# Performance work log

Measured on AMD Instinct MI355X. Metric: run time of the kernel, lower is better.

## Reference

```python
import jax, jax.numpy as jnp
import numpy as np

D = 128          # embed_dim
NSYM = 100000    # num_symbols
PAD = NSYM       # padding idx (zero row)
B = 2048         # query batch
FEW = 5          # support set size
M = 128          # max neighbors
KTAB = 64        # knn table width
K = 32           # knn_k topk
STEPS = 4        # process_steps
DM = 2 * D       # d_model for encoders (256)
HID = 2 * DM     # LSTM hidden (512)


def _cos(a, b):
    # torch F.cosine_similarity, eps=1e-8; a [B,1,d], b [B,N,d] -> [B,N]
    num = jnp.sum(a * b, axis=-1)
    den = jnp.maximum(jnp.linalg.norm(a, axis=-1) * jnp.linalg.norm(b, axis=-1), 1e-8)
    return num / den


def _l2n(x):
    return x / jnp.maximum(jnp.linalg.norm(x, axis=-1, keepdims=True), 1e-12)


def _neighbor_encoder(conn, ids, knn_tab, emb, gcn_w, gcn_w_b, gcn_b, gate_w, gate_b):
    rel = emb[conn[..., 0]]                      # [N,M,D]
    ent = emb[conn[..., 1]]                      # [N,M,D]
    center = emb[ids][:, None, :]                # [N,1,D]
    sim = _cos(center, ent)                      # [N,M]
    _, idx = jax.lax.top_k(sim, K)               # [N,K]
    rel_k = jnp.take_along_axis(rel, idx[..., None], axis=1)
    ent_k = jnp.take_along_axis(ent, idx[..., None], axis=1)
    h = jnp.concatenate([rel_k, ent_k], axis=-1) @ gcn_w.T + gcn_w_b + gcn_b
    struct = jnp.tanh(h.mean(axis=1))            # [N,D]
    # knn branch: gather knn neighbor ids, cosine topk, pad-relation embeds (zero row)
    kent = emb[knn_tab[ids]]                     # [N,KTAB,D]
    sim2 = _cos(center, kent)
    _, idx2 = jax.lax.top_k(sim2, K)
    kent_k = jnp.take_along_axis(kent, idx2[..., None], axis=1)
    pad_row = jax.lax.stop_gradient(emb[PAD])    # padding_idx row (zeros, no grad)
    krel = jnp.broadcast_to(pad_row, kent_k.shape)
    h2 = jnp.concatenate([krel, kent_k], axis=-1) @ gcn_w.T + gcn_w_b + gcn_b
    knn_mean = jnp.tanh(h2.mean(axis=1))         # [N,D]
    alpha = jax.nn.sigmoid(jnp.concatenate([struct, knn_mean], axis=-1) @ gate_w.T + gate_b)
    return (1.0 - alpha) * struct + alpha * knn_mean


def _support_encoder(x, p1_w, p1_b, p2_w, p2_b, ln_g, ln_b):
    o = jax.nn.relu(x @ p1_w.T + p1_b) @ p2_w.T + p2_b
    z = o + x
    mu = z.mean(axis=-1, keepdims=True)
    sig = z.std(axis=-1, ddof=1, keepdims=True)  # torch unbiased std
    return (z - mu) / (sig + 1e-3) * ln_g + ln_b


def _query_encoder(support, query, w_ih, w_hh, b_ih, b_hh):
    # attLSTM processing block; support [1,DM], query [B,DM]
    n = query.shape[0]
    h_r = jnp.zeros((n, HID), query.dtype)
    c = jnp.zeros((n, HID), query.dtype)
    h = query
    for _ in range(STEPS):
        g = query @ w_ih.T + b_ih + h_r @ w_hh.T + b_hh
        i, f, gg, o = jnp.split(g, 4, axis=-1)
        c = jax.nn.sigmoid(f) * c + jax.nn.sigmoid(i) * jnp.tanh(gg)
        h_ = jax.nn.sigmoid(o) * jnp.tanh(c)
        h = query + h_[:, :DM]
        attn = jax.nn.softmax(h @ support.T, axis=1)  # [B,1]
        r = attn @ support                             # [B,DM]
        h_r = jnp.concatenate([h, r], axis=1)
    return h


def _forward(query, support, q_l_conn, q_r_conn, s_l_conn, s_r_conn, knn_neighbors,
             emb, gcn_w, gcn_w_b, gcn_b, gate_w, gate_b,
             p1_w, p1_b, p2_w, p2_b, ln_g, ln_b, w_ih, w_hh, b_ih, b_hh):
    ne = lambda conn, ids: _neighbor_encoder(conn, ids, knn_neighbors, emb,
                                             gcn_w, gcn_w_b, gcn_b, gate_w, gate_b)
    ql = ne(q_l_conn, query[:, 0])
    qr = ne(q_r_conn, query[:, 1])
    sl = ne(s_l_conn, support[:, 0])
    sr = ne(s_r_conn, support[:, 1])
    qn = jnp.concatenate([ql, qr], axis=-1)   # [B,DM]
    sn = jnp.concatenate([sl, sr], axis=-1)   # [FEW,DM]
    se = lambda x: _support_encoder(x, p1_w, p1_b, p2_w, p2_b, ln_g, ln_b)
    support_g = se(sn).mean(axis=0, keepdims=True)  # [1,DM]
    query_g = se(qn)                                 # [B,DM]
    query_f = _l2n(_query_encoder(support_g, query_g, w_ih, w_hh, b_ih, b_hh))
    sg = _l2n(support_g[0])
    return query_f @ sg                              # [B]


def setup_inputs() -> dict:
    key = jax.random.key(0)
    ks = jax.random.split(key, 24)
    f = lambda i, shape, s=0.05: jax.random.normal(ks[i], shape, dtype=jnp.float32) * s
    ri = lambda i, shape: jax.random.randint(ks[i], shape, 0, NSYM).astype(jnp.int32)
    emb = f(0, (NSYM + 1, D), 0.5).at[PAD].set(0.0)
    return dict(
        query=ri(1, (B, 2)), support=ri(2, (FEW, 2)),
        q_l_conn=ri(3, (B, M, 2)),
        q_l_deg=jax.random.randint(ks[4], (B,), 1, M).astype(jnp.int32),
        q_r_conn=ri(5, (B, M, 2)),
        q_r_deg=jax.random.randint(ks[6], (B,), 1, M).astype(jnp.int32),
        s_l_conn=ri(7, (FEW, M, 2)),
        s_l_deg=jax.random.randint(ks[8], (FEW,), 1, M).astype(jnp.int32),
        s_r_conn=ri(9, (FEW, M, 2)),
        s_r_deg=jax.random.randint(ks[10], (FEW,), 1, M).astype(jnp.int32),
        knn_neighbors=ri(11, (NSYM + 1, KTAB)),
        emb=emb,
        gcn_w=f(12, (D, 2 * D)), gcn_w_b=f(13, (D,)),
        gcn_b=jnp.zeros((D,), jnp.float32),
        gate_w=f(14, (1, 2 * D)), gate_b=jnp.zeros((1,), jnp.float32),
        p1_w=f(15, (2 * DM, DM)), p1_b=f(16, (2 * DM,)),
        p2_w=f(17, (DM, 2 * DM)), p2_b=f(18, (DM,)),
        ln_g=jnp.ones((DM,), jnp.float32), ln_b=jnp.zeros((DM,), jnp.float32),
        w_ih=f(19, (4 * HID, DM)), w_hh=f(20, (4 * HID, HID)),
        b_ih=f(21, (4 * HID,)), b_hh=f(22, (4 * HID,)),
    )


def reference(query, support, q_l_conn, q_l_deg, q_r_conn, q_r_deg,
              s_l_conn, s_l_deg, s_r_conn, s_r_deg, knn_neighbors,
              emb, gcn_w, gcn_w_b, gcn_b, gate_w, gate_b,
              p1_w, p1_b, p2_w, p2_b, ln_g, ln_b, w_ih, w_hh, b_ih, b_hh):
    # degrees are computed-but-unused in this fork's neighbor_encoder (plain mean)
    return _forward(query, support, q_l_conn, q_r_conn, s_l_conn, s_r_conn, knn_neighbors,
                    emb, gcn_w, gcn_w_b, gcn_b, gate_w, gate_b,
                    p1_w, p1_b, p2_w, p2_b, ln_g, ln_b, w_ih, w_hh, b_ih, b_hh)
```

## Files before the change

### kernel.cpp

```cpp
#include <hip/hip_runtime.h>
#include <hip/hip_bf16.h>

typedef unsigned short u16;
typedef unsigned int u32;

constexpr int ED   = 128;
constexpr int MC   = 128;
constexpr int KT   = 64;
constexpr int KS   = 32;
constexpr int NB   = 2048;
constexpr int NF   = 5;
constexpr int DMM  = 256;
constexpr int NG   = 1024;
constexpr int PADID = 100000;
constexpr int NROWS = 2*NB + 2*NF;
constexpr int MT   = (NROWS + 63)/64;
constexpr int MP   = MT*64;

typedef __attribute__((ext_vector_type(8))) short short8;
typedef __attribute__((ext_vector_type(4))) float floatx4;

__device__ __forceinline__ float bf2f(u16 u){
  union { u32 i; float f; } v; v.i = ((u32)u) << 16; return v.f;
}
__device__ __forceinline__ float lo2f(u32 w){
  union { u32 i; float f; } v; v.i = w << 16; return v.f;
}
__device__ __forceinline__ float hi2f(u32 w){
  union { u32 i; float f; } v; v.i = w & 0xffff0000u; return v.f;
}
__device__ __forceinline__ u16 f2bf(float f){
  union { float f; u32 i; } v; v.f = f;
  u32 r = v.i + 0x7FFFu + ((v.i >> 16) & 1u);
  return (u16)(r >> 16);
}
__device__ __forceinline__ float sigf(float x){ return 1.f / (1.f + expf(-x)); }

__device__ __forceinline__ bool sniff(const void* ln_g){
  return *(const u32*)ln_g == 0x3F803F80u;
}

__device__ __forceinline__ float gld(const void* p, size_t i, bool bf){
  return bf ? bf2f(((const u16*)p)[i]) : ((const float*)p)[i];
}
__device__ __forceinline__ void ld4(const void* p, size_t i0, bool bf, float* o){
  if (bf){ uint2 w = *(const uint2*)((const u16*)p + i0);
           o[0]=lo2f(w.x); o[1]=hi2f(w.x); o[2]=lo2f(w.y); o[3]=hi2f(w.y); }
  else   { float4 v = *(const float4*)((const float*)p + i0);
           o[0]=v.x; o[1]=v.y; o[2]=v.z; o[3]=v.w; }
}
__device__ __forceinline__ void ld8(const void* p, size_t i0, bool bf, float* o){
  if (bf){
    uint4 v = *(const uint4*)((const u16*)p + i0);
    o[0]=lo2f(v.x); o[1]=hi2f(v.x); o[2]=lo2f(v.y); o[3]=hi2f(v.y);
    o[4]=lo2f(v.z); o[5]=hi2f(v.z); o[6]=lo2f(v.w); o[7]=hi2f(v.w);
  } else {
    const float* f = (const float*)p + i0;
    float4 a = *(const float4*)f, b = *(const float4*)(f + 4);
    o[0]=a.x; o[1]=a.y; o[2]=a.z; o[3]=a.w; o[4]=b.x; o[5]=b.y; o[6]=b.z; o[7]=b.w;
  }
}
__device__ __forceinline__ float dotw(const void* w, size_t i0, const float* x, int n, bool bf){
  float acc = 0.f, t[8];
  #pragma unroll 4
  for (int j = 0; j < n; j += 8){
    ld8(w, i0 + j, bf, t);
    #pragma unroll
    for (int q = 0; q < 8; q++) acc += t[q]*x[j+q];
  }
  return acc;
}

__device__ __forceinline__ float waveSum(float v){
  #pragma unroll
  for (int o = 32; o > 0; o >>= 1) v += __shfl_xor(v, o, 64);
  return v;
}
__device__ __forceinline__ float blockSum(float v, float* s8){
  int lane = threadIdx.x & 63, wid = threadIdx.x >> 6;
  v = waveSum(v);
  __syncthreads();
  if (lane == 0) s8[wid] = v;
  __syncthreads();
  return s8[0] + s8[1] + s8[2] + s8[3];
}
__device__ __forceinline__ float2 blockSum2(float a, float b, float* s8){
  int lane = threadIdx.x & 63, wid = threadIdx.x >> 6;
  a = waveSum(a); b = waveSum(b);
  __syncthreads();
  if (lane == 0){ s8[wid] = a; s8[4 + wid] = b; }
  __syncthreads();
  float2 r;
  r.x = s8[0] + s8[1] + s8[2] + s8[3];
  r.y = s8[4] + s8[5] + s8[6] + s8[7];
  return r;
}

__global__ __launch_bounds__(256) void neighbor_kernel(
    const int* __restrict__ query, const int* __restrict__ support,
    const int* __restrict__ qlc, const int* __restrict__ qrc,
    const int* __restrict__ slc, const int* __restrict__ srcc,
    const int* __restrict__ knnt, const void* __restrict__ emb,
    float* __restrict__ gA, float* __restrict__ gK, const void* __restrict__ ln_g)
{
  const bool bf = sniff(ln_g);
  int blk = blockIdx.x;
  const int* conn; int id;
  if (blk < NB)            { id = query[2*blk];                 conn = qlc + (size_t)blk*MC*2; }
  else if (blk < 2*NB)     { int r = blk - NB;   id = query[2*r+1];   conn = qrc + (size_t)r*MC*2; }
  else if (blk < 2*NB+NF)  { int r = blk - 2*NB; id = support[2*r];   conn = slc + (size_t)r*MC*2; }
  else                     { int r = blk - 2*NB - NF; id = support[2*r+1]; conn = srcc + (size_t)r*MC*2; }

  __shared__ float s_center[ED];
  __shared__ float s_sim[MC + KT];
  __shared__ float s_red[8];
  __shared__ int s_eid[MC + KT];
  __shared__ int s_selE[KS], s_selR[KS], s_selK[KS];

  const int tid = threadIdx.x, lane = tid & 63, wid = tid >> 6;

  if (tid < ED) s_center[tid] = gld(emb, (size_t)id*ED + tid, bf);
  if (tid < MC)           s_eid[tid] = conn[2*tid + 1];
  else if (tid < MC + KT) s_eid[tid] = knnt[(size_t)id*KT + (tid - MC)];

  float cpart = 0.f;
  if (tid < ED){ float c = s_center[tid]; cpart = c*c; }
  float cnorm = sqrtf(blockSum(cpart, s_red));

  const int g = lane & 15;
  float creg[8];
  #pragma unroll
  for (int j = 0; j < 8; j++) creg[j] = s_center[g*8 + j];

  #pragma unroll 4
  for (int m0 = wid*4; m0 < MC + KT; m0 += 16){
    int m = m0 + (lane >> 4);
    int eid = s_eid[m];
    float e[8];
    ld8(emb, (size_t)eid*ED + g*8, bf, e);
    float d = 0.f, q = 0.f;
    #pragma unroll
    for (int j = 0; j < 8; j++){ d += creg[j]*e[j]; q += e[j]*e[j]; }
    #pragma unroll
    for (int o = 8; o > 0; o >>= 1){ d += __shfl_xor(d, o, 64); q += __shfl_xor(q, o, 64); }
    if (g == 0) s_sim[m] = d / fmaxf(cnorm * sqrtf(q), 1e-8f);
  }
  __syncthreads();

  if (tid < MC){
    float v = s_sim[tid];
    int cnt = 0;
    #pragma unroll 8
    for (int j = 0; j < MC; j++){
      float w = s_sim[j];
      cnt += (w > v || (w == v && j < tid)) ? 1 : 0;
    }
    if (cnt < KS){ s_selR[cnt] = conn[2*tid]; s_selE[cnt] = s_eid[tid]; }
  } else if (tid < MC + KT){
    int t = tid - MC;
    float v = s_sim[MC + t];
    int cnt = 0;
    #pragma unroll 8
    for (int j = 0; j < KT; j++){
      float w = s_sim[MC + j];
      cnt += (w > v || (w == v && j < t)) ? 1 : 0;
    }
    if (cnt < KS) s_selK[cnt] = s_eid[MC + t];
  }
  __syncthreads();

  {
    const int slot = tid & 7;
    const int c4 = (tid >> 3) * 4;
    float aR[4] = {0,0,0,0}, aE[4] = {0,0,0,0}, aK[4] = {0,0,0,0};
    #pragma unroll
    for (int k = 0; k < 4; k++){
      float t[4];
      ld4(emb, (size_t)s_selR[k*8 + slot]*ED + c4, bf, t);
      aR[0]+=t[0]; aR[1]+=t[1]; aR[2]+=t[2]; aR[3]+=t[3];
      ld4(emb, (size_t)s_selE[k*8 + slot]*ED + c4, bf, t);
      aE[0]+=t[0]; aE[1]+=t[1]; aE[2]+=t[2]; aE[3]+=t[3];
      ld4(emb, (size_t)s_selK[k*8 + slot]*ED + c4, bf, t);
      aK[0]+=t[0]; aK[1]+=t[1]; aK[2]+=t[2]; aK[3]+=t[3];
    }
    #pragma unroll
    for (int off = 1; off < 8; off <<= 1){
      #pragma unroll
      for (int i = 0; i < 4; i++){
        aR[i] += __shfl_xor(aR[i], off, 64);
        aE[i] += __shfl_xor(aE[i], off, 64);
        aK[i] += __shfl_xor(aK[i], off, 64);
      }
    }
    if (slot == 0){
      constexpr float s = 1.f/KS;
      *(float4*)&gA[(size_t)blk*DMM + c4] =
          make_float4(aR[0]*s, aR[1]*s, aR[2]*s, aR[3]*s);
      *(float4*)&gA[(size_t)blk*DMM + ED + c4] =
          make_float4(aE[0]*s, aE[1]*s, aE[2]*s, aE[3]*s);
      *(float4*)&gK[(size_t)blk*ED + c4] =
          make_float4(aK[0]*s, aK[1]*s, aK[2]*s, aK[3]*s);
    }
  }
}

__global__ __launch_bounds__(256) void gcn_gemm(
    const float* __restrict__ ARE, const float* __restrict__ AK,
    const void* __restrict__ gcn_w, const void* __restrict__ gcn_w_b,
    const void* __restrict__ gcn_b, float* __restrict__ C, const void* __restrict__ ln_g)
{
  const bool bf = sniff(ln_g);
  __shared__ float As2[16][68];
  __shared__ float Ws2[16][68];
  int tid = threadIdx.x;
  int n0 = blockIdx.x * 64;
  int mt = blockIdx.y;
  const float* A; int lda, K, woff; size_t cbase; int mtt;
  if (mt < MT){ A = ARE; lda = DMM; K = DMM; woff = 0;  cbase = 0;              mtt = mt; }
  else        { A = AK;  lda = ED;  K = ED;  woff = ED; cbase = (size_t)MP*ED;  mtt = mt - MT; }
  int m0 = mtt*64;

  int tx = tid & 15, ty = tid >> 4;
  int sn_ = tid & 63, kq = tid >> 6;
  size_t wbase = (size_t)(n0 + sn_)*DMM + woff;
  int ar = tid >> 2, ac = (tid & 3)*4;
  const float* ap = A + (size_t)(m0 + ar)*lda + ac;

  float acc[4][4];
  #pragma unroll
  for (int i = 0; i < 4; i++)
    #pragma unroll
    for (int j = 0; j < 4; j++) acc[i][j] = 0.f;

  for (int kc = 0; kc < K; kc += 16){
    __syncthreads();
    float4 av = *(const float4*)(ap + kc);
    As2[ac+0][ar] = av.x; As2[ac+1][ar] = av.y; As2[ac+2][ar] = av.z; As2[ac+3][ar] = av.w;
    float wt[4];
    ld4(gcn_w, wbase + kc + kq*4, bf, wt);
    Ws2[kq*4+0][sn_] = wt[0]; Ws2[kq*4+1][sn_] = wt[1];
    Ws2[kq*4+2][sn_] = wt[2]; Ws2[kq*4+3][sn_] = wt[3];
    __syncthreads();
    #pragma unroll
    for (int k = 0; k < 16; k++){
      float4 a = *(const float4*)&As2[k][ty*4];
      float4 b = *(const float4*)&Ws2[k][tx*4];
      acc[0][0] += a.x*b.x; acc[0][1] += a.x*b.y; acc[0][2] += a.x*b.z; acc[0][3] += a.x*b.w;
      acc[1][0] += a.y*b.x; acc[1][1] += a.y*b.y; acc[1][2] += a.y*b.z; acc[1][3] += a.y*b.w;
      acc[2][0] += a.z*b.x; acc[2][1] += a.z*b.y; acc[2][2] += a.z*b.z; acc[2][3] += a.z*b.w;
      acc[3][0] += a.w*b.x; acc[3][1] += a.w*b.y; acc[3][2] += a.w*b.z; acc[3][3] += a.w*b.w;
    }
  }

  float b4[4];
  #pragma unroll
  for (int j = 0; j < 4; j++){
    int n = n0 + tx*4 + j;
    b4[j] = gld(gcn_w_b, n, bf) + gld(gcn_b, n, bf);
  }
  #pragma unroll
  for (int i = 0; i < 4; i++){
    int row = m0 + ty*4 + i;
    float4 v = make_float4(acc[i][0]+b4[0], acc[i][1]+b4[1], acc[i][2]+b4[2], acc[i][3]+b4[3]);
    *(float4*)(C + cbase + (size_t)row*ED + n0 + tx*4) = v;
  }
}

__global__ __launch_bounds__(256) void mlp_enc_kernel(
    const float* __restrict__ gC, const void* __restrict__ gate_w,
    const void* __restrict__ gate_b,
    const void* __restrict__ p1_w, const void* __restrict__ p1_b,
    const void* __restrict__ p2_w, const void* __restrict__ p2_b,
    const void* __restrict__ ln_g, const void* __restrict__ ln_b,
    float* __restrict__ dst, int nrows)
{
  const bool bf = sniff(ln_g);
  constexpr int RPB = 8;
  __shared__ float x[RPB][DMM];
  __shared__ float hid[RPB][2*DMM];
  __shared__ float s_red[8];
  int tid = threadIdx.x;
  int r0 = blockIdx.x * RPB;

  {
    int rr = tid >> 5, c4 = (tid & 31) * 4;
    int row = r0 + rr;
    bool valid = row < nrows;
    int rowc = valid ? row : 0;
    int pairL, pairR;
    if (rowc < NB){ pairL = rowc;               pairR = NB + rowc; }
    else          { pairL = 2*NB + (rowc - NB); pairR = 2*NB + NF + (rowc - NB); }
    float4 pl1 = *(const float4*)(gC + (size_t)pairL*ED + c4);
    float4 pl2 = *(const float4*)(gC + (size_t)(MP + pairL)*ED + c4);
    float4 pr1 = *(const float4*)(gC + (size_t)pairR*ED + c4);
    float4 pr2 = *(const float4*)(gC + (size_t)(MP + pairR)*ED + c4);
    float sl[4] = {tanhf(pl1.x), tanhf(pl1.y), tanhf(pl1.z), tanhf(pl1.w)};
    float kl[4] = {tanhf(pl2.x), tanhf(pl2.y), tanhf(pl2.z), tanhf(pl2.w)};
    float sr[4] = {tanhf(pr1.x), tanhf(pr1.y), tanhf(pr1.z), tanhf(pr1.w)};
    float kr[4] = {tanhf(pr2.x), tanhf(pr2.y), tanhf(pr2.z), tanhf(pr2.w)};
    float gwS[4], gwK[4];
    ld4(gate_w, c4, bf, gwS);
    ld4(gate_w, ED + c4, bf, gwK);
    float gvL = 0.f, gvR = 0.f;
    #pragma unroll
    for (int i = 0; i < 4; i++){
      gvL += gwS[i]*sl[i] + gwK[i]*kl[i];
      gvR += gwS[i]*sr[i] + gwK[i]*kr[i];
    }
    #pragma unroll
    for (int o = 16; o > 0; o >>= 1){
      gvL += __shfl_xor(gvL, o, 64);
      gvR += __shfl_xor(gvR, o, 64);
    }
    float gb0 = gld(gate_b, 0, bf);
    float aL = sigf(gvL + gb0), aR = sigf(gvR + gb0);
    float4 xL, xR;
    xL.x = valid ? (1.f-aL)*sl[0] + aL*kl[0] : 0.f;
    xL.y = valid ? (1.f-aL)*sl[1] + aL*kl[1] : 0.f;
    xL.z = valid ? (1.f-aL)*sl[2] + aL*kl[2] : 0.f;
    xL.w = valid ? (1.f-aL)*sl[3] + aL*kl[3] : 0.f;
    xR.x = valid ? (1.f-aR)*sr[0] + aR*kr[0] : 0.f;
    xR.y = valid ? (1.f-aR)*sr[1] + aR*kr[1] : 0.f;
    xR.z = valid ? (1.f-aR)*sr[2] + aR*kr[2] : 0.f;
    xR.w = valid ? (1.f-aR)*sr[3] + aR*kr[3] : 0.f;
    *(float4*)&x[rr][c4]      = xL;
    *(float4*)&x[rr][ED + c4] = xR;
  }
  __syncthreads();

  {
    float acc0[RPB], acc1[RPB];
    #pragma unroll
    for (int r = 0; r < RPB; r++){ acc0[r] = 0.f; acc1[r] = 0.f; }
    for (int j8 = 0; j8 < DMM/8; j8++){
      float wa[8], wb[8];
      ld8(p1_w, (size_t)tid*DMM + j8*8, bf, wa);
      ld8(p1_w, (size_t)(tid+256)*DMM + j8*8, bf, wb);
      #pragma unroll
      for (int r = 0; r < RPB; r++){
        const float* xr = &x[r][j8*8];
        float s0 = 0.f, s1 = 0.f;
        #pragma unroll
        for (int q = 0; q < 8; q++){ float xv = xr[q]; s0 += wa[q]*xv; s1 += wb[q]*xv; }
        acc0[r] += s0; acc1[r] += s1;
      }
    }
    float bb0 = gld(p1_b, tid, bf), bb1 = gld(p1_b, tid + 256, bf);
    #pragma unroll
    for (int r = 0; r < RPB; r++){
      hid[r][tid]     = fmaxf(acc0[r] + bb0, 0.f);
      hid[r][tid+256] = fmaxf(acc1[r] + bb1, 0.f);
    }
  }
  __syncthreads();

  float zr[RPB];
  {
    #pragma unroll
    for (int r = 0; r < RPB; r++) zr[r] = 0.f;
    for (int j8 = 0; j8 < (2*DMM)/8; j8++){
      float wa[8];
      ld8(p2_w, (size_t)tid*(2*DMM) + j8*8, bf, wa);
      #pragma unroll
      for (int r = 0; r < RPB; r++){
        const float* hr = &hid[r][j8*8];
        float s0 = 0.f;
        #pragma unroll
        for (int q = 0; q < 8; q++) s0 += wa[q]*hr[q];
        zr[r] += s0;
      }
    }
    float bb = gld(p2_b, tid, bf);
    #pragma unroll
    for (int r = 0; r < RPB; r++) zr[r] += bb + x[r][tid];
  }

  float lg = gld(ln_g, tid, bf), lb = gld(ln_b, tid, bf);
  for (int r = 0; r < RPB; r++){
    float2 st = blockSum2(zr[r], zr[r]*zr[r], s_red);
    float mu = st.x * (1.f/DMM);
    float var = (st.y - (float)DMM*mu*mu) * (1.f/(DMM - 1));
    float sig = sqrtf(fmaxf(var, 0.f));
    if (r0 + r < nrows)
      dst[(size_t)(r0 + r)*DMM + tid] = (zr[r] - mu)/(sig + 1e-3f)*lg + lb;
  }
}

__global__ __launch_bounds__(256) void prep_kernel(
    const void* __restrict__ w_ih, const void* __restrict__ w_hh,
    const void* __restrict__ b_ih, const void* __restrict__ b_hh,
    const float* __restrict__ seS,
    float* __restrict__ WT_ih, float* __restrict__ WT_hh,
    float* __restrict__ svec, float* __restrict__ cvec0,
    float* __restrict__ sgn, const void* __restrict__ ln_g)
{
  const bool bf = sniff(ln_g);
  const int b = blockIdx.x, tid = threadIdx.x;
  if (b < 32){
    const void* W = (b < 16) ? w_ih : w_hh;
    const int wstride = (b < 16) ? 256 : 512;
    float* WT = (b < 16) ? WT_ih : WT_hh;
    const int n0 = (b & 15) * 64;
    __shared__ float tile[64][65];
    const int nl = tid >> 2, kq = tid & 3;
    const int kl = tid >> 2, nq = tid & 3;
    const int wrow = ((n0 + nl) >> 8)*512 + ((n0 + nl) & 255);
    for (int kc = 0; kc < 256; kc += 64){
      __syncthreads();
      float t[16];
      ld8(W, (size_t)wrow*wstride + kc + kq*16,     bf, t);
      ld8(W, (size_t)wrow*wstride + kc + kq*16 + 8, bf, t + 8);
      #pragma unroll
      for (int i = 0; i < 16; i++) tile[nl][kq*16 + i] = t[i];
      __syncthreads();
      float o[16];
      #pragma unroll
      for (int i = 0; i < 16; i++) o[i] = tile[nq*16 + i][kl];
      #pragma unroll
      for (int i = 0; i < 16; i += 4)
        *(float4*)&WT[(size_t)(kc + kl)*NG + n0 + nq*16 + i] =
            make_float4(o[i], o[i+1], o[i+2], o[i+3]);
    }
  } else {
    const int n0 = (b - 32) * 64;
    __shared__ float sg[DMM];
    __shared__ float part[64][4];
    __shared__ float s_red[8];
    if (tid < DMM){
      float a = 0.f;
      #pragma unroll
      for (int r = 0; r < NF; r++) a += seS[r*DMM + tid];
      sg[tid] = a * (1.f/NF);
    }
    __syncthreads();
    if (b == 32){
      float sq = (tid < DMM) ? sg[tid]*sg[tid] : 0.f;
      float nn = blockSum(sq, s_red);
      if (tid < DMM) sgn[tid] = sg[tid] / fmaxf(sqrtf(nn), 1e-12f);
    }
    const int nl = tid >> 2, q = tid & 3;
    const int n = n0 + nl;
    const int wrow = (n >> 8)*512 + (n & 255);
    float acc = 0.f, t[8];
    #pragma unroll
    for (int k8 = 0; k8 < 8; k8++){
      ld8(w_hh, (size_t)wrow*(2*DMM) + DMM + q*64 + k8*8, bf, t);
      #pragma unroll
      for (int j = 0; j < 8; j++) acc += t[j]*sg[q*64 + k8*8 + j];
    }
    part[nl][q] = acc;
    __syncthreads();
    if (tid < 64){
      svec[n0 + tid] = part[tid][0] + part[tid][1] + part[tid][2] + part[tid][3];
      const int wr2 = ((n0 + tid) >> 8)*512 + ((n0 + tid) & 255);
      cvec0[n0 + tid] = gld(b_ih, wr2, bf) + gld(b_hh, wr2, bf);
    }
  }
}

__global__ __launch_bounds__(256) void gemm_gates(
    const float* __restrict__ A,
    const void* __restrict__ W, const float* __restrict__ WT, int wstride,
    const float* __restrict__ addvec, const float* __restrict__ addmat,
    float* __restrict__ C, const void* __restrict__ ln_g)
{
  const bool bf = sniff(ln_g);
  int tid = threadIdx.x;
  int n0 = blockIdx.x * 64, m0 = blockIdx.y * 64;

  if (bf){
    constexpr int KP = 136;
    __shared__ u16 As[64 * KP];
    __shared__ u16 Ws[64 * KP];
    const int wv = tid >> 6, lane = tid & 63;
    const int quad = lane >> 4, l16 = lane & 15;
    const int sr = tid >> 5, sc = tid & 31;

    floatx4 acc[4];
    #pragma unroll
    for (int t = 0; t < 4; t++) acc[t] = (floatx4){0.f, 0.f, 0.f, 0.f};

    for (int kc = 0; kc < 256; kc += 128){
      __syncthreads();
      #pragma unroll
      for (int i = 0; i < 8; i++){
        int r = i*8 + sr;
        float4 v = *(const float4*)(A + (size_t)(m0 + r)*256 + kc + sc*4);
        u32 p0 = (u32)f2bf(v.x) | ((u32)f2bf(v.y) << 16);
        u32 p1 = (u32)f2bf(v.z) | ((u32)f2bf(v.w) << 16);
        *(uint2*)&As[r*KP + sc*4] = make_uint2(p0, p1);
      }
      #pragma unroll
      for (int i = 0; i < 8; i++){
        int nn = i*8 + sr;
        int gn = n0 + nn;
        int wrow = (gn >> 8)*512 + (gn & 255);
        uint2 wv2 = *(const uint2*)((const u16*)W + (size_t)wrow*wstride + kc + sc*4);
        *(uint2*)&Ws[nn*KP + sc*4] = wv2;
      }
      __syncthreads();
      int am = wv*16 + l16;
      #pragma unroll
      for (int k1 = 0; k1 < 128; k1 += 32){
        int ko = k1 + quad*8;
        short8 af = *(const short8*)&As[am*KP + ko];
        #pragma unroll
        for (int t = 0; t < 4; t++){
          short8 bfr = *(const short8*)&Ws[(t*16 + l16)*KP + ko];
          acc[t] = __builtin_amdgcn_mfma_f32_16x16x32_bf16(af, bfr, acc[t], 0, 0, 0);
        }
      }
    }

    #pragma unroll
    for (int t = 0; t < 4; t++){
      int col = n0 + t*16 + l16;
      float av = addvec ? addvec[col] : 0.f;
      #pragma unroll
      for (int r = 0; r < 4; r++){
        int row = m0 + wv*16 + quad*4 + r;
        float val = acc[t][r] + av;
        if (addmat) val += addmat[(size_t)row*NG + col];
        C[(size_t)row*NG + col] = val;
      }
    }
    return;
  }

  {
    __shared__ float As2[32][68];
    __shared__ float Ws2[32][68];
    int tx = tid & 15, ty = tid >> 4;
    int arow = tid >> 2, acol = (tid & 3) * 8;
    int wkr = tid >> 3, wnc = (tid & 7) * 8;
    const float* ap = A + (size_t)(m0 + arow)*256 + acol;
    const float* wp = WT + (size_t)wkr*NG + n0 + wnc;

    float acc[4][4];
    #pragma unroll
    for (int i = 0; i < 4; i++)
      #pragma unroll
      for (int j = 0; j < 4; j++) acc[i][j] = 0.f;

    for (int kc = 0; kc < 256; kc += 32){
      __syncthreads();
      float4 a0 = *(const float4*)(ap + kc);
      float4 a1 = *(const float4*)(ap + kc + 4);
      As2[acol+0][arow] = a0.x; As2[acol+1][arow] = a0.y;
      As2[acol+2][arow] = a0.z; As2[acol+3][arow] = a0.w;
      As2[acol+4][arow] = a1.x; As2[acol+5][arow] = a1.y;
      As2[acol+6][arow] = a1.z; As2[acol+7][arow] = a1.w;
      float4 w0 = *(const float4*)(wp + (size_t)kc*NG);
      float4 w1 = *(const float4*)(wp + (size_t)kc*NG + 4);
      *(float4*)&Ws2[wkr][wnc]     = w0;
      *(float4*)&Ws2[wkr][wnc + 4] = w1;
      __syncthreads();
      #pragma unroll
      for (int k = 0; k < 32; k++){
        float4 a = *(const float4*)&As2[k][ty*4];
        float4 b = *(const float4*)&Ws2[k][tx*4];
        acc[0][0] += a.x*b.x; acc[0][1] += a.x*b.y; acc[0][2] += a.x*b.z; acc[0][3] += a.x*b.w;
        acc[1][0] += a.y*b.x; acc[1][1] += a.y*b.y; acc[1][2] += a.y*b.z; acc[1][3] += a.y*b.w;
        acc[2][0] += a.z*b.x; acc[2][1] += a.z*b.y; acc[2][2] += a.z*b.z; acc[2][3] += a.z*b.w;
        acc[3][0] += a.w*b.x; acc[3][1] += a.w*b.y; acc[3][2] += a.w*b.z; acc[3][3] += a.w*b.w;
      }
    }

    float4 addc = make_float4(0.f, 0.f, 0.f, 0.f);
    if (addvec){
      float4 t = *(const float4*)(addvec + n0 + tx*4);
      addc.x = t.x; addc.y = t.y; addc.z = t.z; addc.w = t.w;
    }
    #pragma unroll
    for (int i = 0; i < 4; i++){
      int row = m0 + ty*4 + i;
      float4 v = make_float4(acc[i][0]+addc.x, acc[i][1]+addc.y, acc[i][2]+addc.z, acc[i][3]+addc.w);
      if (addmat){
        float4 t = *(const float4*)(addmat + (size_t)row*NG + n0 + tx*4);
        v.x += t.x; v.y += t.y; v.z += t.z; v.w += t.w;
      }
      *(float4*)(C + (size_t)row*NG + n0 + tx*4) = v;
    }
  }
}

__global__ __launch_bounds__(256) void lstm_elem(
    const float* __restrict__ g, const float* __restrict__ query_g,
    float* __restrict__ c, float* __restrict__ h, int first,
    const float* __restrict__ sgn, void* __restrict__ out, const void* __restrict__ ln_g)
{
  __shared__ float s_red[8];
  int b = blockIdx.x, j = threadIdx.x;
  const float* gb = g + (size_t)b*NG;
  float iv = gb[j], fv = gb[256 + j], gv = gb[512 + j], ov = gb[768 + j];
  float cc = first ? 0.f : c[(size_t)b*DMM + j];
  cc = sigf(fv)*cc + sigf(iv)*tanhf(gv);
  c[(size_t)b*DMM + j] = cc;
  float hh = query_g[(size_t)b*DMM + j] + sigf(ov)*tanhf(cc);
  h[(size_t)b*DMM + j] = hh;
  if (out){
    float2 st = blockSum2(hh*sgn[j], hh*hh, s_red);
    if (j == 0){
      float v = st.x / fmaxf(sqrtf(st.y), 1e-12f);
      if (sniff(ln_g)) ((__hip_bfloat16*)out)[b] = __float2bfloat16(v);
      else             ((float*)out)[b] = v;
    }
  }
}

extern "C" void kernel_launch(void* const* d_in, const int* in_sizes, int n_in,
                              void* d_out, int out_size, void* d_ws, size_t ws_size,
                              hipStream_t stream)
{
  const int* query   = (const int*)d_in[0];
  const int* support = (const int*)d_in[1];
  const int* qlc     = (const int*)d_in[2];
  const int* qrc     = (const int*)d_in[4];
  const int* slc     = (const int*)d_in[6];
  const int* srcc    = (const int*)d_in[8];
  const int* knnt    = (const int*)d_in[10];
  const void* emb     = d_in[11];
  const void* gcn_w   = d_in[12];
  const void* gcn_w_b = d_in[13];
  const void* gcn_b   = d_in[14];
  const void* gate_w  = d_in[15];
  const void* gate_b  = d_in[16];
  const void* p1_w    = d_in[17];
  const void* p1_b    = d_in[18];
  const void* p2_w    = d_in[19];
  const void* p2_b    = d_in[20];
  const void* ln_g    = d_in[21];
  const void* ln_b    = d_in[22];
  const void* w_ih    = d_in[23];
  const void* w_hh    = d_in[24];
  const void* b_ih    = d_in[25];
  const void* b_hh    = d_in[26];

  float* ws = (float*)d_ws + 64;
  size_t off = 0;
  float* query_g = ws + off; off += (size_t)NB*DMM;
  float* seS     = ws + off; off += NF*DMM;
  float* sgn     = ws + off; off += DMM;
  float* cvec0   = ws + off; off += NG;
  float* svec    = ws + off; off += NG;
  float* qx      = ws + off; off += (size_t)NB*NG;
  float* gbuf    = ws + off; off += (size_t)NB*NG;
  float* hbuf    = ws + off; off += (size_t)NB*DMM;
  float* cbuf    = ws + off; off += (size_t)NB*DMM;
  float* WT_ih   = ws + off; off += (size_t)DMM*NG;
  float* WT_hh   = ws + off; off += (size_t)DMM*NG;
  float* gA      = ws + off; off += (size_t)MP*DMM;
  float* gK      = ws + off; off += (size_t)MP*ED;
  float* gC      = ws + off; off += (size_t)2*MP*ED;

  neighbor_kernel<<<NROWS, 256, 0, stream>>>(
      query, support, qlc, qrc, slc, srcc, knnt, emb, gA, gK, ln_g);

  gcn_gemm<<<dim3(2, 2*MT), 256, 0, stream>>>(gA, gK, gcn_w, gcn_w_b, gcn_b, gC, ln_g);

  mlp_enc_kernel<<<(NB + NF + 7)/8, 256, 0, stream>>>(
      gC, gate_w, gate_b, p1_w, p1_b, p2_w, p2_b, ln_g, ln_b, query_g, NB + NF);

  prep_kernel<<<48, 256, 0, stream>>>(
      w_ih, w_hh, b_ih, b_hh, seS, WT_ih, WT_hh, svec, cvec0, sgn, ln_g);

  gemm_gates<<<dim3(NG/64, NB/64), 256, 0, stream>>>(
      query_g, w_ih, WT_ih, 256, cvec0, nullptr, qx, ln_g);

  lstm_elem<<<NB, 256, 0, stream>>>(qx, query_g, cbuf, hbuf, 1, nullptr, nullptr, ln_g);
  for (int s = 1; s < 4; s++){
    gemm_gates<<<dim3(NG/64, NB/64), 256, 0, stream>>>(
        hbuf, w_hh, WT_hh, 512, svec, qx, gbuf, ln_g);
    lstm_elem<<<NB, 256, 0, stream>>>(gbuf, query_g, cbuf, hbuf, 0,
                                      sgn, (s == 3) ? d_out : nullptr, ln_g);
  }

  (void)in_sizes; (void)n_in; (void)out_size; (void)ws_size;
}
```

Measured before the change: 433.7 us.

## Fuse LSTM cell update into gate GEMM epilogue and interleave gate columns

Reorders the gate GEMM's output columns so each block computes the i/f/g/o gates for the same 16 hidden units. That lets the LSTM cell and hidden update run in the GEMM epilogue, which removes the separate elementwise kernel and the full gate buffer write and read per step. Hidden state now ping-pongs between two buffers, and a small cosine kernel produces the final output. The neighbor kernel's reduction also changes from shuffle-based to shared-memory partial sums with coalesced stores.

```diff
diff --git a/kernel.cpp b/kernel.cpp
--- a/kernel.cpp
+++ b/kernel.cpp
@@ -116,6 +116,7 @@
   __shared__ float s_red[8];
   __shared__ int s_eid[MC + KT];
   __shared__ int s_selE[KS], s_selR[KS], s_selK[KS];
+  __shared__ float s_mt[3][8][ED];
 
   const int tid = threadIdx.x, lane = tid & 63, wid = tid >> 6;
 
@@ -170,8 +171,7 @@
   __syncthreads();
 
   {
-    const int slot = tid & 7;
-    const int c4 = (tid >> 3) * 4;
+    const int slot = tid >> 5, c4 = (tid & 31)*4;
     float aR[4] = {0,0,0,0}, aE[4] = {0,0,0,0}, aK[4] = {0,0,0,0};
     #pragma unroll
     for (int k = 0; k < 4; k++){
@@ -183,23 +183,22 @@
       ld4(emb, (size_t)s_selK[k*8 + slot]*ED + c4, bf, t);
       aK[0]+=t[0]; aK[1]+=t[1]; aK[2]+=t[2]; aK[3]+=t[3];
     }
-    #pragma unroll
-    for (int off = 1; off < 8; off <<= 1){
-      #pragma unroll
-      for (int i = 0; i < 4; i++){
-        aR[i] += __shfl_xor(aR[i], off, 64);
-        aE[i] += __shfl_xor(aE[i], off, 64);
-        aK[i] += __shfl_xor(aK[i], off, 64);
-      }
-    }
-    if (slot == 0){
-      constexpr float s = 1.f/KS;
-      *(float4*)&gA[(size_t)blk*DMM + c4] =
-          make_float4(aR[0]*s, aR[1]*s, aR[2]*s, aR[3]*s);
-      *(float4*)&gA[(size_t)blk*DMM + ED + c4] =
-          make_float4(aE[0]*s, aE[1]*s, aE[2]*s, aE[3]*s);
-      *(float4*)&gK[(size_t)blk*ED + c4] =
-          make_float4(aK[0]*s, aK[1]*s, aK[2]*s, aK[3]*s);
+    *(float4*)&s_mt[0][slot][c4] = make_float4(aR[0], aR[1], aR[2], aR[3]);
+    *(float4*)&s_mt[1][slot][c4] = make_float4(aE[0], aE[1], aE[2], aE[3]);
+    *(float4*)&s_mt[2][slot][c4] = make_float4(aK[0], aK[1], aK[2], aK[3]);
+  }
+  __syncthreads();
+  {
+    int dd = tid & (ED - 1), which = tid >> 7;
+    float s = 0.f;
+    #pragma unroll
+    for (int p = 0; p < 8; p++) s += s_mt[which][p][dd];
+    gA[(size_t)blk*DMM + which*ED + dd] = s * (1.f/KS);
+    if (tid < ED){
+      float sk = 0.f;
+      #pragma unroll
+      for (int p = 0; p < 8; p++) sk += s_mt[2][p][dd];
+      gK[(size_t)blk*ED + dd] = sk * (1.f/KS);
     }
   }
 }
@@ -462,11 +461,13 @@
     const float* __restrict__ A,
     const void* __restrict__ W, const float* __restrict__ WT, int wstride,
     const float* __restrict__ addvec, const float* __restrict__ addmat,
-    float* __restrict__ C, const void* __restrict__ ln_g)
+    float* __restrict__ C, float* __restrict__ cst,
+    float* __restrict__ hout, const float* __restrict__ qg,
+    int fuse, const void* __restrict__ ln_g)
 {
   const bool bf = sniff(ln_g);
   int tid = threadIdx.x;
-  int n0 = blockIdx.x * 64, m0 = blockIdx.y * 64;
+  int jb0 = blockIdx.x * 16, m0 = blockIdx.y * 64;
 
   if (bf){
     constexpr int KP = 136;
@@ -493,8 +494,7 @@
       #pragma unroll
       for (int i = 0; i < 8; i++){
         int nn = i*8 + sr;
-        int gn = n0 + nn;
-        int wrow = (gn >> 8)*512 + (gn & 255);
+        int wrow = (nn >> 4)*512 + jb0 + (nn & 15);
         uint2 wv2 = *(const uint2*)((const u16*)W + (size_t)wrow*wstride + kc + sc*4);
         *(uint2*)&Ws[nn*KP + sc*4] = wv2;
       }
@@ -512,29 +512,43 @@
       }
     }
 
+    float val[4][4];
     #pragma unroll
     for (int t = 0; t < 4; t++){
-      int col = n0 + t*16 + l16;
+      int col = t*256 + jb0 + l16;
       float av = addvec ? addvec[col] : 0.f;
       #pragma unroll
       for (int r = 0; r < 4; r++){
         int row = m0 + wv*16 + quad*4 + r;
-        float val = acc[t][r] + av;
-        if (addmat) val += addmat[(size_t)row*NG + col];
-        C[(size_t)row*NG + col] = val;
+        float v = acc[t][r] + av;
+        if (addmat) v += addmat[(size_t)row*NG + col];
+        val[t][r] = v;
+        if (C) C[(size_t)row*NG + col] = v;
+      }
+    }
+    if (fuse){
+      #pragma unroll
+      for (int r = 0; r < 4; r++){
+        int row = m0 + wv*16 + quad*4 + r;
+        int j = jb0 + l16;
+        float cc = (fuse == 2) ? 0.f : cst[(size_t)row*DMM + j];
+        cc = sigf(val[1][r])*cc + sigf(val[0][r])*tanhf(val[2][r]);
+        cst[(size_t)row*DMM + j] = cc;
+        hout[(size_t)row*DMM + j] = qg[(size_t)row*DMM + j] + sigf(val[3][r])*tanhf(cc);
       }
     }
     return;
   }
 
   {
-    __shared__ float As2[32][68];
-    __shared__ float Ws2[32][68];
+    __shared__ float smem2[2*32*68];
+    float (*As2)[68] = (float(*)[68])smem2;
+    float (*Ws2)[68] = (float(*)[68])(smem2 + 32*68);
     int tx = tid & 15, ty = tid >> 4;
     int arow = tid >> 2, acol = (tid & 3) * 8;
-    int wkr = tid >> 3, wnc = (tid & 7) * 8;
+    int wkr = tid >> 3, oct = tid & 7;
     const float* ap = A + (size_t)(m0 + arow)*256 + acol;
-    const float* wp = WT + (size_t)wkr*NG + n0 + wnc;
+    const float* wp = WT + (size_t)(oct >> 1)*256 + jb0 + (oct & 1)*8;
 
     float acc[4][4];
     #pragma unroll
@@ -550,10 +564,11 @@
       As2[acol+2][arow] = a0.z; As2[acol+3][arow] = a0.w;
       As2[acol+4][arow] = a1.x; As2[acol+5][arow] = a1.y;
       As2[acol+6][arow] = a1.z; As2[acol+7][arow] = a1.w;
-      float4 w0 = *(const float4*)(wp + (size_t)kc*NG);
-      float4 w1 = *(const float4*)(wp + (size_t)kc*NG + 4);
-      *(float4*)&Ws2[wkr][wnc]     = w0;
-      *(float4*)&Ws2[wkr][wnc + 4] = w1;
+      const float* wrow_p = wp + (size_t)(kc + wkr)*NG;
+      float4 w0 = *(const float4*)(wrow_p);
+      float4 w1 = *(const float4*)(wrow_p + 4);
+      *(float4*)&Ws2[wkr][oct*8]     = w0;
+      *(float4*)&Ws2[wkr][oct*8 + 4] = w1;
       __syncthreads();
       #pragma unroll
       for (int k = 0; k < 32; k++){
@@ -566,45 +581,64 @@
       }
     }
 
+    int gate = (tx*4) >> 4;
+    int ncol = gate*256 + jb0 + ((tx*4) & 15);
     float4 addc = make_float4(0.f, 0.f, 0.f, 0.f);
     if (addvec){
-      float4 t = *(const float4*)(addvec + n0 + tx*4);
+      float4 t = *(const float4*)(addvec + ncol);
       addc.x = t.x; addc.y = t.y; addc.z = t.z; addc.w = t.w;
     }
+    float val[4][4];
     #pragma unroll
     for (int i = 0; i < 4; i++){
       int row = m0 + ty*4 + i;
       float4 v = make_float4(acc[i][0]+addc.x, acc[i][1]+addc.y, acc[i][2]+addc.z, acc[i][3]+addc.w);
       if (addmat){
-        float4 t = *(const float4*)(addmat + (size_t)row*NG + n0 + tx*4);
+        float4 t = *(const float4*)(addmat + (size_t)row*NG + ncol);
         v.x += t.x; v.y += t.y; v.z += t.z; v.w += t.w;
       }
-      *(float4*)(C + (size_t)row*NG + n0 + tx*4) = v;
-    }
-  }
-}
-
-__global__ __launch_bounds__(256) void lstm_elem(
-    const float* __restrict__ g, const float* __restrict__ query_g,
-    float* __restrict__ c, float* __restrict__ h, int first,
-    const float* __restrict__ sgn, void* __restrict__ out, const void* __restrict__ ln_g)
+      val[i][0] = v.x; val[i][1] = v.y; val[i][2] = v.z; val[i][3] = v.w;
+      if (C) *(float4*)(C + (size_t)row*NG + ncol) = v;
+    }
+
+    if (fuse){
+      __syncthreads();
+      float (*epi)[65] = (float(*)[65])smem2;
+      #pragma unroll
+      for (int i = 0; i < 4; i++)
+        *(float4*)&epi[ty*4 + i][tx*4] = make_float4(val[i][0], val[i][1], val[i][2], val[i][3]);
+      __syncthreads();
+      int j_local = tid & 15, rg = tid >> 4;
+      #pragma unroll
+      for (int rr = 0; rr < 4; rr++){
+        int row_l = rg*4 + rr;
+        int row = m0 + row_l;
+        int j = jb0 + j_local;
+        float iv = epi[row_l][j_local];
+        float fv = epi[row_l][16 + j_local];
+        float gv = epi[row_l][32 + j_local];
+        float ov = epi[row_l][48 + j_local];
+        float cc = (fuse == 2) ? 0.f : cst[(size_t)row*DMM + j];
+        cc = sigf(fv)*cc + sigf(iv)*tanhf(gv);
+        cst[(size_t)row*DMM + j] = cc;
+        hout[(size_t)row*DMM + j] = qg[(size_t)row*DMM + j] + sigf(ov)*tanhf(cc);
+      }
+    }
+  }
+}
+
+__global__ __launch_bounds__(256) void cosine_kernel(
+    const float* __restrict__ h, const float* __restrict__ sgn,
+    void* __restrict__ out, const void* __restrict__ ln_g)
 {
   __shared__ float s_red[8];
   int b = blockIdx.x, j = threadIdx.x;
-  const float* gb = g + (size_t)b*NG;
-  float iv = gb[j], fv = gb[256 + j], gv = gb[512 + j], ov = gb[768 + j];
-  float cc = first ? 0.f : c[(size_t)b*DMM + j];
-  cc = sigf(fv)*cc + sigf(iv)*tanhf(gv);
-  c[(size_t)b*DMM + j] = cc;
-  float hh = query_g[(size_t)b*DMM + j] + sigf(ov)*tanhf(cc);
-  h[(size_t)b*DMM + j] = hh;
-  if (out){
-    float2 st = blockSum2(hh*sgn[j], hh*hh, s_red);
-    if (j == 0){
-      float v = st.x / fmaxf(sqrtf(st.y), 1e-12f);
-      if (sniff(ln_g)) ((__hip_bfloat16*)out)[b] = __float2bfloat16(v);
-      else             ((float*)out)[b] = v;
-    }
+  float hh = h[(size_t)b*DMM + j];
+  float2 st = blockSum2(hh*sgn[j], hh*hh, s_red);
+  if (j == 0){
+    float v = st.x / fmaxf(sqrtf(st.y), 1e-12f);
+    if (sniff(ln_g)) ((__hip_bfloat16*)out)[b] = __float2bfloat16(v);
+    else             ((float*)out)[b] = v;
   }
 }
 
@@ -644,8 +678,8 @@
   float* cvec0   = ws + off; off += NG;
   float* svec    = ws + off; off += NG;
   float* qx      = ws + off; off += (size_t)NB*NG;
-  float* gbuf    = ws + off; off += (size_t)NB*NG;
-  float* hbuf    = ws + off; off += (size_t)NB*DMM;
+  float* hA      = ws + off; off += (size_t)NB*DMM;
+  float* hB      = ws + off; off += (size_t)NB*DMM;
   float* cbuf    = ws + off; off += (size_t)NB*DMM;
   float* WT_ih   = ws + off; off += (size_t)DMM*NG;
   float* WT_hh   = ws + off; off += (size_t)DMM*NG;
@@ -664,16 +698,19 @@
   prep_kernel<<<48, 256, 0, stream>>>(
       w_ih, w_hh, b_ih, b_hh, seS, WT_ih, WT_hh, svec, cvec0, sgn, ln_g);
 
-  gemm_gates<<<dim3(NG/64, NB/64), 256, 0, stream>>>(
-      query_g, w_ih, WT_ih, 256, cvec0, nullptr, qx, ln_g);
-
-  lstm_elem<<<NB, 256, 0, stream>>>(qx, query_g, cbuf, hbuf, 1, nullptr, nullptr, ln_g);
+  gemm_gates<<<dim3(16, NB/64), 256, 0, stream>>>(
+      query_g, w_ih, WT_ih, 256, cvec0, nullptr, qx,
+      cbuf, hA, query_g, 2, ln_g);
+
+  float* hin = hA; float* hout2 = hB;
   for (int s = 1; s < 4; s++){
-    gemm_gates<<<dim3(NG/64, NB/64), 256, 0, stream>>>(
-        hbuf, w_hh, WT_hh, 512, svec, qx, gbuf, ln_g);
-    lstm_elem<<<NB, 256, 0, stream>>>(gbuf, query_g, cbuf, hbuf, 0,
-                                      sgn, (s == 3) ? d_out : nullptr, ln_g);
-  }
+    gemm_gates<<<dim3(16, NB/64), 256, 0, stream>>>(
+        hin, w_hh, WT_hh, 512, svec, qx, nullptr,
+        cbuf, hout2, query_g, 1, ln_g);
+    float* tmp = hin; hin = hout2; hout2 = tmp;
+  }
+
+  cosine_kernel<<<NB, 256, 0, stream>>>(hin, sgn, d_out, ln_g);
 
   (void)in_sizes; (void)n_in; (void)out_size; (void)ws_size;
 }
```

New measurement: 425.1 us. 1.02x faster.
